# Optimization experiments

Measured on AMD Instinct MI355X. Metric: run time of the kernel, lower is better.

The kernel has to match this reference:

```python
import jax, jax.numpy as jnp
import numpy as np

EMBED = 1024
HEADS = 16
HEAD_DIM = EMBED // HEADS


def setup_inputs() -> dict:
    key = jax.random.key(0)
    ks = jax.random.split(key, 10)
    B, S = 2, 2048
    x = jax.random.normal(ks[0], (B, S, EMBED), dtype=jnp.float32)
    s = 1.0 / np.sqrt(EMBED)
    Wq = jax.random.normal(ks[1], (EMBED, EMBED), dtype=jnp.float32) * s
    Wk = jax.random.normal(ks[2], (EMBED, EMBED), dtype=jnp.float32) * s
    Wv = jax.random.normal(ks[3], (EMBED, EMBED), dtype=jnp.float32) * s
    Wo = jax.random.normal(ks[4], (EMBED, EMBED), dtype=jnp.float32) * s
    bq = jnp.zeros((EMBED,), jnp.float32)
    bk = jnp.zeros((EMBED,), jnp.float32)
    bv = jnp.zeros((EMBED,), jnp.float32)
    bo = jnp.zeros((EMBED,), jnp.float32)
    J = jax.random.normal(ks[5], (HEADS, HEAD_DIM, HEAD_DIM), dtype=jnp.float32) * 0.02
    lam = jnp.asarray(0.5, jnp.float32)
    return {"x": x, "Wq": Wq, "bq": bq, "Wk": Wk, "bk": bk,
            "Wv": Wv, "bv": bv, "Wo": Wo, "bo": bo, "J": J, "lam": lam}


def reference(x, Wq, bq, Wk, bk, Wv, bv, Wo, bo, J, lam):
    B, S, E = x.shape
    H, hd = HEADS, HEAD_DIM
    scale = np.sqrt(hd).astype(np.float32)

    def split_heads(t):  # (B,S,E) -> (B,H,S,hd)
        return t.reshape(B, S, H, hd).transpose(0, 2, 1, 3)

    Q = split_heads(x @ Wq + bq)
    K = split_heads(x @ Wk + bk)
    V = split_heads(x @ Wv + bv)

    scores = jnp.einsum('bhid,bhjd->bhij', Q, K) / scale
    Qn = jnp.tanh(Q)
    Kn = jnp.tanh(K)
    # bilinear correction: tanh(Q) J tanh(K)^T per head
    delta = jnp.einsum('bhid,hde,bhje->bhij', Qn, J, Kn)
    scores = scores + lam * delta

    causal = jnp.triu(jnp.ones((S, S), dtype=bool), k=1)  # True above diagonal
    scores = jnp.where(causal[None, None], -jnp.inf, scores)

    probs = jax.nn.softmax(scores, axis=-1)
    out = jnp.einsum('bhij,bhjd->bhid', probs, V)
    out = out.transpose(0, 2, 1, 3).reshape(B, S, E)
    return out @ Wo + bo
```

## Files before the change

### kernel.cpp

```cpp
#include <hip/hip_runtime.h>
#include <cstdint>
#include <cstddef>

typedef __bf16 bf16x8 __attribute__((ext_vector_type(8)));
typedef short  s16x8  __attribute__((ext_vector_type(8)));
typedef float  f32x4  __attribute__((ext_vector_type(4)));
typedef unsigned int u32x4 __attribute__((ext_vector_type(4)));

#define MFMA16(a, b, c) __builtin_amdgcn_mfma_f32_16x16x32_bf16((a), (b), (c), 0, 0, 0)

typedef __attribute__((address_space(3))) unsigned int       lds_uint;
typedef const __attribute__((address_space(1))) unsigned int glb_uint;

static __device__ __forceinline__ void gload_lds16(const void* g, void* l) {
  __builtin_amdgcn_global_load_lds((glb_uint*)g, (lds_uint*)l, 16, 0, 0);
}

static __device__ __forceinline__ unsigned short f2bf(float f) {
  unsigned u = __builtin_bit_cast(unsigned, f);
  unsigned r = u + 0x7FFFu + ((u >> 16) & 1u);
  return (unsigned short)(r >> 16);
}
static __device__ __forceinline__ float bf2f(unsigned short u) {
  unsigned x = ((unsigned)u) << 16;
  return __builtin_bit_cast(float, x);
}
static __device__ __forceinline__ float fast_tanh(float x) {
  float e = __expf(2.f * x);
  return 1.f - 2.f / (e + 1.f);
}
static __device__ __forceinline__ unsigned cvt_pk_bf16(float lo, float hi) {
  unsigned r;
  asm("v_cvt_pk_bf16_f32 %0, %1, %2" : "=v"(r) : "v"(lo), "v"(hi));
  return r;
}

__global__ void k_f32_to_bf16(const float* __restrict__ src,
                              unsigned short* __restrict__ dst, int n4) {
  int i = blockIdx.x * blockDim.x + threadIdx.x;
  if (i >= n4) return;
  float4 v = reinterpret_cast<const float4*>(src)[i];
  ushort4 o;
  o.x = f2bf(v.x); o.y = f2bf(v.y); o.z = f2bf(v.z); o.w = f2bf(v.w);
  reinterpret_cast<ushort4*>(dst)[i] = o;
}

__global__ void k_transpose_to_bf16(const float* __restrict__ src,
                                    unsigned short* __restrict__ dst,
                                    int Rr, int Cc) {
  __shared__ float t[32][33];
  int c0 = blockIdx.x * 32, r0 = blockIdx.y * 32;
  int tx = threadIdx.x, ty = threadIdx.y;
#pragma unroll
  for (int i = 0; i < 4; ++i)
    t[ty + i * 8][tx] = src[(size_t)(r0 + ty + i * 8) * Cc + c0 + tx];
  __syncthreads();
#pragma unroll
  for (int i = 0; i < 4; ++i)
    dst[(size_t)(c0 + ty + i * 8) * Rr + r0 + tx] = f2bf(t[tx][ty + i * 8]);
}

template <int MODE>
__global__ __launch_bounds__(256) void k_gemm(
    const unsigned short* __restrict__ A, const unsigned short* __restrict__ Bt,
    int M, int N, int K,
    float* __restrict__ Cout, const float* __restrict__ bias) {
  __shared__ __align__(16) unsigned short Al[128 * 64];
  __shared__ __align__(16) unsigned short Bl[128 * 64];
  const int tid = threadIdx.x;
  const int lane = tid & 63, w = tid >> 6;
  const int wm = w >> 1, wn = w & 1;
  const int l15 = lane & 15, l4 = lane >> 4;
  const int m0 = blockIdx.y * 128, n0 = blockIdx.x * 128;

  const int srow = lane >> 3;
  const int schunk = (lane & 7) ^ srow;
  const unsigned short* Ag = A + (size_t)(m0 + (w << 5) + srow) * K + (schunk << 3);
  const unsigned short* Bg = Bt + (size_t)(n0 + (w << 5) + srow) * K + (schunk << 3);
  unsigned short* Alw = Al + (w << 5) * 64;
  unsigned short* Blw = Bl + (w << 5) * 64;

  const f32x4 zero4 = {0.f, 0.f, 0.f, 0.f};
  f32x4 acc[4][4];
#pragma unroll
  for (int i = 0; i < 4; ++i)
#pragma unroll
    for (int j = 0; j < 4; ++j) acc[i][j] = zero4;

  for (int k0 = 0; k0 < K; k0 += 64) {
#pragma unroll
    for (int p = 0; p < 4; ++p) {
      gload_lds16(Ag + (size_t)(p * 8) * K + k0, Alw + p * 8 * 64);
      gload_lds16(Bg + (size_t)(p * 8) * K + k0, Blw + p * 8 * 64);
    }
    __syncthreads();
#pragma unroll
    for (int c = 0; c < 2; ++c) {
      bf16x8 af[4], bfr[4];
#pragma unroll
      for (int i = 0; i < 4; ++i) {
        int ra = wm * 64 + i * 16 + l15;
        af[i] = *reinterpret_cast<const bf16x8*>(
            reinterpret_cast<const char*>(Al) + ra * 128 +
            ((c * 64 + l4 * 16) ^ ((ra & 7) << 4)));
        int rb = wn * 64 + i * 16 + l15;
        bfr[i] = *reinterpret_cast<const bf16x8*>(
            reinterpret_cast<const char*>(Bl) + rb * 128 +
            ((c * 64 + l4 * 16) ^ ((rb & 7) << 4)));
      }
#pragma unroll
      for (int i = 0; i < 4; ++i)
#pragma unroll
        for (int j = 0; j < 4; ++j) acc[i][j] = MFMA16(af[i], bfr[j], acc[i][j]);
    }
    __syncthreads();
  }

#pragma unroll
  for (int i = 0; i < 4; ++i)
#pragma unroll
    for (int j = 0; j < 4; ++j)
#pragma unroll
      for (int r = 0; r < 4; ++r) {
        int mrow = m0 + wm * 64 + i * 16 + l4 * 4 + r;
        int ncol = n0 + wn * 64 + j * 16 + l15;
        Cout[(size_t)mrow * N + ncol] = acc[i][j][r] + bias[ncol];
      }
}

__global__ __launch_bounds__(512, 2) void k_gemm256_qkv(
    const unsigned short* __restrict__ A, const unsigned short* __restrict__ Bt,
    int M, int N, int K,
    const float* __restrict__ bq, const float* __restrict__ bk,
    const float* __restrict__ bv,
    unsigned short* __restrict__ Qa, unsigned short* __restrict__ Ka,
    unsigned short* __restrict__ Vt, unsigned short* __restrict__ Qn) {
  __shared__ __align__(16) unsigned short Al[2][256 * 64];
  __shared__ __align__(16) unsigned short Bl[2][256 * 64];
  const int tid = threadIdx.x;
  const int lane = tid & 63;
  const int w = tid >> 6, wm = w >> 2, wn = w & 3;
  const int l15 = lane & 15, l4 = lane >> 4;
  const int nbx = N >> 8;
  const int bid = (int)blockIdx.x;
  const int lin = (bid & 7) * ((int)gridDim.x >> 3) + (bid >> 3);
  const int m0 = (lin / nbx) << 8, n0 = (lin % nbx) << 8;
  const int NT = K >> 6;

  const int strow = tid >> 3, stchunk = tid & 7;
  const int schunk = stchunk ^ (strow & 7);

  auto stage = [&](int slot, int kt, int hh) {
    const unsigned short* src = (hh < 2) ? A : Bt;
    const int base0 = (hh < 2) ? m0 : n0;
    unsigned short* dst = (hh < 2) ? &Al[slot][0] : &Bl[slot][0];
    const int hrow = (hh & 1) * 128;
#pragma unroll
    for (int i = 0; i < 2; ++i) {
      int row = hrow + i * 64 + strow;
      gload_lds16(src + (size_t)(base0 + row) * K + kt * 64 + schunk * 8,
                  dst + row * 64 + stchunk * 8);
    }
  };

  const f32x4 zero4 = {0.f, 0.f, 0.f, 0.f};
  f32x4 acc[8][4];
#pragma unroll
  for (int i = 0; i < 8; ++i)
#pragma unroll
    for (int j = 0; j < 4; ++j) acc[i][j] = zero4;

  stage(0, 0, 0); stage(0, 0, 1); stage(0, 0, 2); stage(0, 0, 3);
  stage(1, 1, 0);
  asm volatile("s_waitcnt vmcnt(2)" ::: "memory");
  __builtin_amdgcn_s_barrier();

  bf16x8 af[4][2], bf0[2][2], bf1[2][2];

  for (int kt = 0; kt < NT; ++kt) {
    const int s = kt & 1;
    const char* As = (const char*)&Al[s][0];
    const char* Bs = (const char*)&Bl[s][0];
    const int kp1 = (kt + 1 < NT) ? kt + 1 : NT - 1;
    const int kp2 = (kt + 2 < NT) ? kt + 2 : NT - 1;

#pragma unroll
    for (int i = 0; i < 4; ++i) {
      const int ra = wm * 128 + i * 16 + l15;
#pragma unroll
      for (int kk = 0; kk < 2; ++kk)
        af[i][kk] = *(const bf16x8*)(As + ra * 128 + (((kk * 4 + l4) ^ (ra & 7)) << 4));
    }
#pragma unroll
    for (int j = 0; j < 2; ++j) {
      const int rb = wn * 64 + j * 16 + l15;
#pragma unroll
      for (int kk = 0; kk < 2; ++kk)
        bf0[j][kk] = *(const bf16x8*)(Bs + rb * 128 + (((kk * 4 + l4) ^ (rb & 7)) << 4));
    }
    stage(s ^ 1, kp1, 1);
    __builtin_amdgcn_s_barrier();
    asm volatile("s_waitcnt lgkmcnt(0)" ::: "memory");
    __builtin_amdgcn_sched_barrier(0);
    __builtin_amdgcn_s_setprio(1);
#pragma unroll
    for (int i = 0; i < 4; ++i)
#pragma unroll
      for (int j = 0; j < 2; ++j)
#pragma unroll
        for (int kk = 0; kk < 2; ++kk)
          acc[i][j] = MFMA16(af[i][kk], bf0[j][kk], acc[i][j]);
    __builtin_amdgcn_s_setprio(0);
    __builtin_amdgcn_s_barrier();

#pragma unroll
    for (int j = 0; j < 2; ++j) {
      const int rb = wn * 64 + (2 + j) * 16 + l15;
#pragma unroll
      for (int kk = 0; kk < 2; ++kk)
        bf1[j][kk] = *(const bf16x8*)(Bs + rb * 128 + (((kk * 4 + l4) ^ (rb & 7)) << 4));
    }
    stage(s ^ 1, kp1, 2);
    __builtin_amdgcn_s_barrier();
    asm volatile("s_waitcnt lgkmcnt(0)" ::: "memory");
    __builtin_amdgcn_sched_barrier(0);
    __builtin_amdgcn_s_setprio(1);
#pragma unroll
    for (int i = 0; i < 4; ++i)
#pragma unroll
      for (int j = 0; j < 2; ++j)
#pragma unroll
        for (int kk = 0; kk < 2; ++kk)
          acc[i][2 + j] = MFMA16(af[i][kk], bf1[j][kk], acc[i][2 + j]);
    __builtin_amdgcn_s_setprio(0);
    __builtin_amdgcn_s_barrier();

#pragma unroll
    for (int i = 0; i < 4; ++i) {
      const int ra = wm * 128 + (4 + i) * 16 + l15;
#pragma unroll
      for (int kk = 0; kk < 2; ++kk)
        af[i][kk] = *(const bf16x8*)(As + ra * 128 + (((kk * 4 + l4) ^ (ra & 7)) << 4));
    }
    stage(s ^ 1, kp1, 3);
    __builtin_amdgcn_s_barrier();
    asm volatile("s_waitcnt lgkmcnt(0)" ::: "memory");
    __builtin_amdgcn_sched_barrier(0);
    __builtin_amdgcn_s_setprio(1);
#pragma unroll
    for (int i = 0; i < 4; ++i)
#pragma unroll
      for (int j = 0; j < 2; ++j)
#pragma unroll
        for (int kk = 0; kk < 2; ++kk)
          acc[4 + i][2 + j] = MFMA16(af[i][kk], bf1[j][kk], acc[4 + i][2 + j]);
    __builtin_amdgcn_s_setprio(0);
    __builtin_amdgcn_s_barrier();

    stage(s, kp2, 0);
    asm volatile("s_waitcnt vmcnt(2)" ::: "memory");
    __builtin_amdgcn_s_barrier();
    __builtin_amdgcn_s_setprio(1);
#pragma unroll
    for (int i = 0; i < 4; ++i)
#pragma unroll
      for (int j = 0; j < 2; ++j)
#pragma unroll
        for (int kk = 0; kk < 2; ++kk)
          acc[4 + i][j] = MFMA16(af[i][kk], bf0[j][kk], acc[4 + i][j]);
    __builtin_amdgcn_s_setprio(0);
    __builtin_amdgcn_s_barrier();
  }
  asm volatile("s_waitcnt vmcnt(0)" ::: "memory");

#pragma unroll
  for (int mf = 0; mf < 8; ++mf) {
#pragma unroll
    for (int nf = 0; nf < 4; ++nf) {
#pragma unroll
      for (int r = 0; r < 4; ++r) {
        const int mrow = m0 + wm * 128 + mf * 16 + l4 * 4 + r;
        const int ncol = n0 + wn * 64 + nf * 16 + l15;
        const float v = acc[mf][nf][r];
        const int proj = ncol >> 10, nn = ncol & 1023;
        const int h = nn >> 6, d = nn & 63;
        const int b = mrow >> 11, sq = mrow & 2047;
        const size_t t64 = (size_t)(b * 16 + h) * 2048 + sq;
        if (proj == 0) {
          float q = v + bq[nn];
          Qa[t64 * 128 + d] = f2bf(q * 0.125f);
          Qn[t64 * 64 + d] = f2bf(fast_tanh(q));
        } else if (proj == 1) {
          float kk = v + bk[nn];
          Ka[t64 * 128 + d] = f2bf(kk);
          Ka[t64 * 128 + 64 + d] = f2bf(fast_tanh(kk));
        } else {
          Vt[((size_t)(b * 16 + h) * 64 + d) * 2048 + sq] = f2bf(v + bv[nn]);
        }
      }
    }
  }
}

__global__ __launch_bounds__(256) void k_qnj(const unsigned short* __restrict__ Qn,
                                             const float* __restrict__ J,
                                             const float* __restrict__ lamPtr,
                                             unsigned short* __restrict__ Qa) {
  __shared__ float Jl[64 * 64];
  __shared__ float Ql[64 * 64];
  int bid = blockIdx.x;
  int bh = bid >> 5, sblk = bid & 31;
  int h = bh & 15;
  int tid = threadIdx.x;
  float lam = lamPtr[0];
  const float4* Jh = reinterpret_cast<const float4*>(J + (size_t)h * 4096);
#pragma unroll
  for (int p = 0; p < 4; ++p)
    reinterpret_cast<float4*>(Jl)[p * 256 + tid] = Jh[p * 256 + tid];
  size_t tok0 = (size_t)bh * 2048 + sblk * 64;
#pragma unroll
  for (int p = 0; p < 2; ++p) {
    int idx = p * 256 + tid;
    s16x8 v = *reinterpret_cast<const s16x8*>(Qn + tok0 * 64 + idx * 8);
#pragma unroll
    for (int j = 0; j < 8; ++j) Ql[idx * 8 + j] = bf2f((unsigned short)v[j]);
  }
  __syncthreads();
  int e = tid & 63, wq = tid >> 6;
#pragma unroll 1
  for (int pass = 0; pass < 16; ++pass) {
    int tok = pass * 4 + wq;
    float a0 = 0.f, a1 = 0.f;
#pragma unroll
    for (int d = 0; d < 64; d += 2) {
      a0 += Ql[tok * 64 + d] * Jl[d * 64 + e];
      a1 += Ql[tok * 64 + d + 1] * Jl[(d + 1) * 64 + e];
    }
    Qa[(tok0 + tok) * 128 + 64 + e] = f2bf(lam * (a0 + a1));
  }
}

__global__ __launch_bounds__(256) void k_attn(const unsigned short* __restrict__ Qa,
                                              const unsigned short* __restrict__ Ka,
                                              const unsigned short* __restrict__ Vt,
                                              unsigned short* __restrict__ Ob) {
  constexpr int S = 2048;
  __shared__ __align__(16) unsigned short Klds[2][64 * 128];
  __shared__ __align__(16) unsigned short Vtl[2][64 * 64];

  const int blk = (int)blockIdx.x;
  const int xg = blk & 7, idx = blk >> 3;
  const int bh = xg * 4 + (idx & 3);
  const int qt = 31 - (idx >> 2);
  const int b = bh >> 4, h = bh & 15;
  const int tid = threadIdx.x;
  const int lane = tid & 63, w = tid >> 6;
  const int l15 = lane & 15, l4 = lane >> 4;
  const int q0 = qt * 64;
  const size_t bhS = (size_t)bh * S;
  const unsigned short* Kbase = Ka + bhS * 128;
  const unsigned short* Vbase = Vt + (size_t)bh * 64 * 2048;
  const f32x4 zero4 = {0.f, 0.f, 0.f, 0.f};

  const int rowbase = w * 16 + (lane >> 4);
  const int rb7 = rowbase & 7;
  const int cK0 = (lane & 15) ^ rb7;
  const int cK1 = cK0 ^ 4;
  const int vdvrow = w * 16 + (lane >> 3);
  const int cV = (lane & 7) ^ ((lane >> 3) & 7);

  bf16x8 qf[4];
  {
    int qrow = q0 + w * 16 + l15;
#pragma unroll
    for (int c = 0; c < 4; ++c)
      qf[c] = *reinterpret_cast<const bf16x8*>(Qa + (bhS + qrow) * 128 + c * 32 + l4 * 8);
  }

  f32x4 oacc[4];
  float m_ = -__builtin_inff(), lsum = 0.f;
#pragma unroll
  for (int v = 0; v < 4; ++v) oacc[v] = zero4;

  const int I0 = (l15 + 32 * (l4 & 1)) * 4;
  const int I1 = I0 + 64;
  const bool hi4 = (lane & 32) != 0;

#pragma unroll
  for (int p = 0; p < 4; ++p)
    gload_lds16(Kbase + (size_t)(rowbase + 4 * p) * 128 + ((p & 1) ? cK1 : cK0) * 8,
                &Klds[0][(w * 16 + p * 4) * 128]);
#pragma unroll
  for (int p = 0; p < 2; ++p)
    gload_lds16(Vbase + (size_t)(vdvrow + 8 * p) * 2048 + cV * 8,
                &Vtl[0][(w * 16 + p * 8) * 64]);
  __syncthreads();

  for (int kt = 0; kt <= qt; ++kt) {
    const int cur = kt & 1;
    const bool lastStep = (kt == qt);

    if (!lastStep) {
      const int base = (kt + 1) * 64;
      const int nxt = cur ^ 1;
#pragma unroll
      for (int p = 0; p < 4; ++p)
        gload_lds16(Kbase + (size_t)(base + rowbase + 4 * p) * 128 + ((p & 1) ? cK1 : cK0) * 8,
                    &Klds[nxt][(w * 16 + p * 4) * 128]);
#pragma unroll
      for (int p = 0; p < 2; ++p)
        gload_lds16(Vbase + (size_t)(vdvrow + 8 * p) * 2048 + base + cV * 8,
                    &Vtl[nxt][(w * 16 + p * 8) * 64]);
    }

    const char* Kl = reinterpret_cast<const char*>(Klds[cur]);
    f32x4 sc[4];
    __builtin_amdgcn_s_setprio(1);
#pragma unroll
    for (int fn = 0; fn < 4; ++fn) {
      sc[fn] = zero4;
      const int krow = fn * 16 + l15;
#pragma unroll
      for (int c = 0; c < 4; ++c) {
        bf16x8 kf = *reinterpret_cast<const bf16x8*>(
            Kl + krow * 256 + (((c * 4 + l4) ^ (krow & 7)) << 4));
        sc[fn] = MFMA16(kf, qf[c], sc[fn]);
      }
    }
    __builtin_amdgcn_s_setprio(0);

    if (lastStep) {
      const int qloc = w * 16 + l15;
#pragma unroll
      for (int fn = 0; fn < 4; ++fn)
#pragma unroll
        for (int r = 0; r < 4; ++r)
          if (fn * 16 + l4 * 4 + r > qloc) sc[fn][r] = -__builtin_inff();
    }

    float mx = sc[0][0];
#pragma unroll
    for (int fn = 0; fn < 4; ++fn)
#pragma unroll
      for (int r = 0; r < 4; ++r) mx = fmaxf(mx, sc[fn][r]);
    mx = fmaxf(mx, __shfl_xor(mx, 16));
    mx = fmaxf(mx, __shfl_xor(mx, 32));
    const float mn = fmaxf(m_, mx);
    const float al = __expf(m_ - mn);
    float p_[4][4];
    float rs = 0.f;
#pragma unroll
    for (int fn = 0; fn < 4; ++fn)
#pragma unroll
      for (int r = 0; r < 4; ++r) {
        float e = __expf(sc[fn][r] - mn);
        p_[fn][r] = e;
        rs += e;
      }
    rs += __shfl_xor(rs, 16);
    rs += __shfl_xor(rs, 32);
    lsum = lsum * al + rs;
    m_ = mn;

#pragma unroll
    for (int r = 0; r < 4; ++r) {
      float albc = __shfl(al, l4 * 4 + r);
#pragma unroll
      for (int v = 0; v < 4; ++v) oacc[v][r] *= albc;
    }

    unsigned cp[4][2];
#pragma unroll
    for (int fn = 0; fn < 4; ++fn) {
      cp[fn][0] = cvt_pk_bf16(p_[fn][0], p_[fn][1]);
      cp[fn][1] = cvt_pk_bf16(p_[fn][2], p_[fn][3]);
    }

    const char* Vl = reinterpret_cast<const char*>(Vtl[cur]);
#pragma unroll
    for (int c2 = 0; c2 < 2; ++c2) {
      unsigned a0 = __builtin_amdgcn_ds_bpermute(I0, (int)cp[c2 * 2][0]);
      unsigned b0 = __builtin_amdgcn_ds_bpermute(I0, (int)cp[c2 * 2 + 1][0]);
      unsigned a1 = __builtin_amdgcn_ds_bpermute(I0, (int)cp[c2 * 2][1]);
      unsigned b1 = __builtin_amdgcn_ds_bpermute(I0, (int)cp[c2 * 2 + 1][1]);
      unsigned a2 = __builtin_amdgcn_ds_bpermute(I1, (int)cp[c2 * 2][0]);
      unsigned b2 = __builtin_amdgcn_ds_bpermute(I1, (int)cp[c2 * 2 + 1][0]);
      unsigned a3 = __builtin_amdgcn_ds_bpermute(I1, (int)cp[c2 * 2][1]);
      unsigned b3 = __builtin_amdgcn_ds_bpermute(I1, (int)cp[c2 * 2 + 1][1]);
      u32x4 pw = {hi4 ? b0 : a0, hi4 ? b1 : a1, hi4 ? b2 : a2, hi4 ? b3 : a3};
      bf16x8 pa = __builtin_bit_cast(bf16x8, pw);
      __builtin_amdgcn_s_setprio(1);
#pragma unroll
      for (int v = 0; v < 4; ++v) {
        const int dvrow = v * 16 + l15;
        bf16x8 vf = *reinterpret_cast<const bf16x8*>(
            Vl + dvrow * 128 + (((c2 * 4 + l4) ^ (dvrow & 7)) << 4));
        oacc[v] = MFMA16(pa, vf, oacc[v]);
      }
      __builtin_amdgcn_s_setprio(0);
    }

    __syncthreads();
  }

  float lbc[4];
#pragma unroll
  for (int r = 0; r < 4; ++r) lbc[r] = __shfl(lsum, l4 * 4 + r);
#pragma unroll
  for (int v = 0; v < 4; ++v) {
#pragma unroll
    for (int r = 0; r < 4; ++r) {
      int row = q0 + w * 16 + l4 * 4 + r;
      float o = oacc[v][r] / lbc[r];
      Ob[((size_t)b * S + row) * 1024 + h * 64 + v * 16 + l15] = f2bf(o);
    }
  }
}

extern "C" void kernel_launch(void* const* d_in, const int* in_sizes, int n_in,
                              void* d_out, int out_size, void* d_ws, size_t ws_size,
                              hipStream_t stream) {
  const float* x   = (const float*)d_in[0];
  const float* Wq  = (const float*)d_in[1];
  const float* bq  = (const float*)d_in[2];
  const float* Wk  = (const float*)d_in[3];
  const float* bk  = (const float*)d_in[4];
  const float* Wv  = (const float*)d_in[5];
  const float* bv  = (const float*)d_in[6];
  const float* Wo  = (const float*)d_in[7];
  const float* bo  = (const float*)d_in[8];
  const float* J   = (const float*)d_in[9];
  const float* lam = (const float*)d_in[10];
  float* out = (float*)d_out;

  char* ws = (char*)d_ws;
  unsigned short* xb     = (unsigned short*)(ws);
  unsigned short* Wt_qkv = (unsigned short*)(ws + 8388608);
  unsigned short* Wt_o   = (unsigned short*)(ws + 14680064);
  unsigned short* Qa     = (unsigned short*)(ws + 16777216);
  unsigned short* Ka     = (unsigned short*)(ws + 33554432);
  unsigned short* Vt     = (unsigned short*)(ws + 50331648);
  unsigned short* Qn     = (unsigned short*)(ws + 58720256);
  unsigned short* Ob     = (unsigned short*)(ws + 67108864);

  k_f32_to_bf16<<<4096, 256, 0, stream>>>(x, xb, 1048576);

  dim3 tb(32, 8), tg(32, 32);
  k_transpose_to_bf16<<<tg, tb, 0, stream>>>(Wq, Wt_qkv + 0,       1024, 1024);
  k_transpose_to_bf16<<<tg, tb, 0, stream>>>(Wk, Wt_qkv + 1048576, 1024, 1024);
  k_transpose_to_bf16<<<tg, tb, 0, stream>>>(Wv, Wt_qkv + 2097152, 1024, 1024);
  k_transpose_to_bf16<<<tg, tb, 0, stream>>>(Wo, Wt_o,             1024, 1024);

  k_gemm256_qkv<<<192, 512, 0, stream>>>(xb, Wt_qkv, 4096, 3072, 1024,
      bq, bk, bv, Qa, Ka, Vt, Qn);

  k_qnj<<<1024, 256, 0, stream>>>(Qn, J, lam, Qa);

  k_attn<<<1024, 256, 0, stream>>>(Qa, Ka, Vt, Ob);

  k_gemm<0><<<dim3(8, 32), 256, 0, stream>>>(Ob, Wt_o, 4096, 1024, 1024,
      out, bo);
}
```

Before: 196.6 us.

## Prefetch whole next K-tile in QKV GEMM and batch weight transposes

The QKV GEMM main loop now issues every stage of the k+1 tile in the prologue and every stage of the k+2 tile in a single burst before the last MFMA phase. It waits with vmcnt(8) after that phase, replacing loads spread across the four compute phases. This deepens the global-to-LDS prefetch so memory latency hides behind more MFMA work, at the cost of more loads in flight. Separately, the four weight transpose launches are merged into one 3D-grid launch to cut launch overhead.

Result: no change. 195.4 us (-0.6%).

```diff
diff --git a/kernel.cpp b/kernel.cpp
--- a/kernel.cpp
+++ b/kernel.cpp
@@ -45,19 +45,24 @@
   reinterpret_cast<ushort4*>(dst)[i] = o;
 }
 
-__global__ void k_transpose_to_bf16(const float* __restrict__ src,
-                                    unsigned short* __restrict__ dst,
-                                    int Rr, int Cc) {
+__global__ void k_transpose4_to_bf16(const float* __restrict__ s0,
+                                     const float* __restrict__ s1,
+                                     const float* __restrict__ s2,
+                                     const float* __restrict__ s3,
+                                     unsigned short* __restrict__ dstBase) {
   __shared__ float t[32][33];
+  const int z = blockIdx.z;
+  const float* src = (z == 0) ? s0 : (z == 1) ? s1 : (z == 2) ? s2 : s3;
+  unsigned short* dst = dstBase + (size_t)z * 1048576;
   int c0 = blockIdx.x * 32, r0 = blockIdx.y * 32;
   int tx = threadIdx.x, ty = threadIdx.y;
 #pragma unroll
   for (int i = 0; i < 4; ++i)
-    t[ty + i * 8][tx] = src[(size_t)(r0 + ty + i * 8) * Cc + c0 + tx];
+    t[ty + i * 8][tx] = src[(size_t)(r0 + ty + i * 8) * 1024 + c0 + tx];
   __syncthreads();
 #pragma unroll
   for (int i = 0; i < 4; ++i)
-    dst[(size_t)(c0 + ty + i * 8) * Rr + r0 + tx] = f2bf(t[tx][ty + i * 8]);
+    dst[(size_t)(c0 + ty + i * 8) * 1024 + r0 + tx] = f2bf(t[tx][ty + i * 8]);
 }
 
 template <int MODE>
@@ -171,8 +176,8 @@
     for (int j = 0; j < 4; ++j) acc[i][j] = zero4;
 
   stage(0, 0, 0); stage(0, 0, 1); stage(0, 0, 2); stage(0, 0, 3);
-  stage(1, 1, 0);
-  asm volatile("s_waitcnt vmcnt(2)" ::: "memory");
+  stage(1, 1, 0); stage(1, 1, 1); stage(1, 1, 2); stage(1, 1, 3);
+  asm volatile("s_waitcnt vmcnt(8)" ::: "memory");
   __builtin_amdgcn_s_barrier();
 
   bf16x8 af[4][2], bf0[2][2], bf1[2][2];
@@ -181,7 +186,6 @@
     const int s = kt & 1;
     const char* As = (const char*)&Al[s][0];
     const char* Bs = (const char*)&Bl[s][0];
-    const int kp1 = (kt + 1 < NT) ? kt + 1 : NT - 1;
     const int kp2 = (kt + 2 < NT) ? kt + 2 : NT - 1;
 
 #pragma unroll
@@ -198,7 +202,6 @@
       for (int kk = 0; kk < 2; ++kk)
         bf0[j][kk] = *(const bf16x8*)(Bs + rb * 128 + (((kk * 4 + l4) ^ (rb & 7)) << 4));
     }
-    stage(s ^ 1, kp1, 1);
     __builtin_amdgcn_s_barrier();
     asm volatile("s_waitcnt lgkmcnt(0)" ::: "memory");
     __builtin_amdgcn_sched_barrier(0);
@@ -220,7 +223,6 @@
       for (int kk = 0; kk < 2; ++kk)
         bf1[j][kk] = *(const bf16x8*)(Bs + rb * 128 + (((kk * 4 + l4) ^ (rb & 7)) << 4));
     }
-    stage(s ^ 1, kp1, 2);
     __builtin_amdgcn_s_barrier();
     asm volatile("s_waitcnt lgkmcnt(0)" ::: "memory");
     __builtin_amdgcn_sched_barrier(0);
@@ -242,7 +244,6 @@
       for (int kk = 0; kk < 2; ++kk)
         af[i][kk] = *(const bf16x8*)(As + ra * 128 + (((kk * 4 + l4) ^ (ra & 7)) << 4));
     }
-    stage(s ^ 1, kp1, 3);
     __builtin_amdgcn_s_barrier();
     asm volatile("s_waitcnt lgkmcnt(0)" ::: "memory");
     __builtin_amdgcn_sched_barrier(0);
@@ -257,9 +258,8 @@
     __builtin_amdgcn_s_setprio(0);
     __builtin_amdgcn_s_barrier();
 
-    stage(s, kp2, 0);
-    asm volatile("s_waitcnt vmcnt(2)" ::: "memory");
-    __builtin_amdgcn_s_barrier();
+    stage(s, kp2, 0); stage(s, kp2, 1); stage(s, kp2, 2); stage(s, kp2, 3);
+    __builtin_amdgcn_sched_barrier(0);
     __builtin_amdgcn_s_setprio(1);
 #pragma unroll
     for (int i = 0; i < 4; ++i)
@@ -269,6 +269,7 @@
         for (int kk = 0; kk < 2; ++kk)
           acc[4 + i][j] = MFMA16(af[i][kk], bf0[j][kk], acc[4 + i][j]);
     __builtin_amdgcn_s_setprio(0);
+    asm volatile("s_waitcnt vmcnt(8)" ::: "memory");
     __builtin_amdgcn_s_barrier();
   }
   asm volatile("s_waitcnt vmcnt(0)" ::: "memory");
@@ -545,11 +546,8 @@
 
   k_f32_to_bf16<<<4096, 256, 0, stream>>>(x, xb, 1048576);
 
-  dim3 tb(32, 8), tg(32, 32);
-  k_transpose_to_bf16<<<tg, tb, 0, stream>>>(Wq, Wt_qkv + 0,       1024, 1024);
-  k_transpose_to_bf16<<<tg, tb, 0, stream>>>(Wk, Wt_qkv + 1048576, 1024, 1024);
-  k_transpose_to_bf16<<<tg, tb, 0, stream>>>(Wv, Wt_qkv + 2097152, 1024, 1024);
-  k_transpose_to_bf16<<<tg, tb, 0, stream>>>(Wo, Wt_o,             1024, 1024);
+  k_transpose4_to_bf16<<<dim3(32, 32, 4), dim3(32, 8), 0, stream>>>(
+      Wq, Wk, Wv, Wo, Wt_qkv);
 
   k_gemm256_qkv<<<192, 512, 0, stream>>>(xb, Wt_qkv, 4096, 3072, 1024,
       bq, bk, bv, Qa, Ka, Vt, Qn);
```
